# Kernel optimization log

Measured on AMD Instinct MI355X. Metric: run time of the kernel, lower is better.

## Reference

```python
import jax, jax.numpy as jnp
import numpy as np

NUM_HEADS = 8
CH_PER_HEAD = 32
NUM_GROUPS = 32
EPS = 1e-5
SCALE = CH_PER_HEAD ** (-0.25)


def setup_inputs() -> dict:
    key = jax.random.key(0)
    ks = jax.random.split(key, 6)
    B, C, H, W = 2, 256, 64, 64
    hid = NUM_HEADS * CH_PER_HEAD  # 256
    s = 1.0 / np.sqrt(C)
    return {
        "x": jax.random.normal(ks[0], (B, C, H, W), dtype=jnp.float32),
        "gamma": jnp.ones((C,), jnp.float32),
        "beta": jnp.zeros((C,), jnp.float32),
        "wq": jax.random.normal(ks[1], (hid, C), jnp.float32) * s,
        "bq": jnp.zeros((hid,), jnp.float32),
        "wk": jax.random.normal(ks[2], (hid, C), jnp.float32) * s,
        "bk": jnp.zeros((hid,), jnp.float32),
        "wv": jax.random.normal(ks[3], (hid, C), jnp.float32) * s,
        "bv": jnp.zeros((hid,), jnp.float32),
        "wout": jax.random.normal(ks[4], (C, hid), jnp.float32) * s,
        "bout": jnp.zeros((C,), jnp.float32),
    }


def _group_norm(x, gamma, beta):
    b, c, h, w = x.shape
    xg = x.reshape(b, NUM_GROUPS, c // NUM_GROUPS, h, w)
    mu = jnp.mean(xg, axis=(2, 3, 4), keepdims=True)
    var = jnp.var(xg, axis=(2, 3, 4), keepdims=True)
    xg = (xg - mu) * jax.lax.rsqrt(var + EPS)
    return xg.reshape(b, c, h, w) * gamma[None, :, None, None] + beta[None, :, None, None]


def reference(x, gamma, beta, wq, bq, wk, bk, wv, bv, wout, bout):
    b, c, h, w = x.shape
    n = h * w
    x_n = _group_norm(x, gamma, beta).reshape(b, c, n)  # b c n (self-attention: embedding = x_n)
    # 1x1 convs == pointwise linear over the channel dim
    q = jnp.einsum('oc,bcn->bon', wq, x_n) + bq[None, :, None]
    k = jnp.einsum('oc,bcn->bon', wk, x_n) + bk[None, :, None]
    v = jnp.einsum('oc,bcn->bon', wv, x_n) + bv[None, :, None]
    # split heads: b (h d) n -> b h d n
    d = CH_PER_HEAD
    q = q.reshape(b, NUM_HEADS, d, n)
    k = k.reshape(b, NUM_HEADS, d, n)
    v = v.reshape(b, NUM_HEADS, d, n)
    attn = jax.nn.softmax(jnp.einsum('bhdi,bhdj->bhij', q * SCALE, k * SCALE), axis=-1)
    out = jnp.einsum('bhij,bhdj->bhdi', attn, v).reshape(b, NUM_HEADS * d, n)
    out = jnp.einsum('oc,bcn->bon', wout, out) + bout[None, :, None]
    out = out.reshape(b, -1, h, w)
    return x + out  # shapes match -> residual
```

## Files before the change

### kernel.cpp

```cpp
#include <hip/hip_runtime.h>
#include <hip/hip_bf16.h>
#include <stdint.h>

typedef unsigned short u16;
typedef float f32x4 __attribute__((ext_vector_type(4)));
typedef float f32x16 __attribute__((ext_vector_type(16)));
typedef short bf16x8 __attribute__((ext_vector_type(8)));

#define NSP 4096
#define CDIM 256
#define HID 256
#define NH 8
#define DH 32
#define NG 32
#define CPG 8
#define BATCH 2
#define SPLIT 4
#define GN_EPS 1e-5f
#define QK2_SCALE 0.25503488f

#define MFMA32(A, B, C) __builtin_amdgcn_mfma_f32_32x32x16_bf16(A, B, C, 0, 0, 0)
#define MFMA16(A, B, C) __builtin_amdgcn_mfma_f32_16x16x32_bf16(A, B, C, 0, 0, 0)

__device__ __forceinline__ float bf2f(u16 u) {
    union { uint32_t i; float f; } v; v.i = ((uint32_t)u) << 16; return v.f;
}
__device__ __forceinline__ u16 f2bf(float f) {
    union { float f; uint32_t i; } v; v.f = f;
    uint32_t b = v.i;
    return (u16)((b + 0x7FFFu + ((b >> 16) & 1u)) >> 16);
}

__device__ __forceinline__ void gload16(const u16* g, u16* lds) {
    __builtin_amdgcn_global_load_lds(
        (const __attribute__((address_space(1))) uint32_t*)g,
        (__attribute__((address_space(3))) uint32_t*)lds, 16, 0, 0);
}

__device__ __forceinline__ void pl32swap(uint32_t& a, uint32_t& b) {
    asm("v_permlane32_swap_b32 %0, %1" : "+v"(a), "+v"(b));
}

__global__ void gn_stats(const float* __restrict__ x, float* __restrict__ stats,
                         const float* __restrict__ wq, const float* __restrict__ wk,
                         const float* __restrict__ wv, const float* __restrict__ wout,
                         u16* __restrict__ wcat) {
    int blk = blockIdx.x;
#pragma unroll
    for (int i = 0; i < 16; i++) {
        int idx = blk * 4096 + i * 256 + threadIdx.x;
        const float* src = (idx < 65536) ? wq : (idx < 131072) ? wk : (idx < 196608) ? wv : wout;
        wcat[idx] = f2bf(src[idx & 65535]);
    }
    const float4* base = (const float4*)(x + (size_t)blk * (CPG * NSP));
    float s = 0.f, ss = 0.f;
    for (int i = threadIdx.x; i < (CPG * NSP) / 4; i += 256) {
        float4 v = base[i];
        s  += v.x + v.y + v.z + v.w;
        ss += v.x * v.x + v.y * v.y + v.z * v.z + v.w * v.w;
    }
    for (int m = 1; m < 64; m <<= 1) { s += __shfl_xor(s, m, 64); ss += __shfl_xor(ss, m, 64); }
    __shared__ float ls[4], lss[4];
    int w = threadIdx.x >> 6;
    if ((threadIdx.x & 63) == 0) { ls[w] = s; lss[w] = ss; }
    __syncthreads();
    if (threadIdx.x == 0) {
        float S = ls[0] + ls[1] + ls[2] + ls[3];
        float SS = lss[0] + lss[1] + lss[2] + lss[3];
        float mean = S / (float)(CPG * NSP);
        float var = SS / (float)(CPG * NSP) - mean * mean;
        stats[2 * blk] = mean;
        stats[2 * blk + 1] = rsqrtf(var + GN_EPS);
    }
}

__global__ void gn_apply(const float* __restrict__ x, const float* __restrict__ stats,
                         const float* __restrict__ gamma, const float* __restrict__ beta,
                         u16* __restrict__ xn) {
    __shared__ u16 tile[64][72];
    int n0 = blockIdx.x * 64, c0 = blockIdx.y * 64, b = blockIdx.z;
    int t = threadIdx.x;
    int nl = t & 63, cq = t >> 6;
#pragma unroll
    for (int i = 0; i < 16; i++) {
        int cl = i * 4 + cq;
        int c = c0 + cl;
        int g = c >> 3;
        float mean = stats[2 * (b * NG + g)];
        float rstd = stats[2 * (b * NG + g) + 1];
        float v = x[((size_t)b * CDIM + c) * NSP + n0 + nl];
        v = (v - mean) * rstd * gamma[c] + beta[c];
        tile[cl][nl] = f2bf(v);
    }
    __syncthreads();
    int nr = t >> 2, cc = (t & 3) * 16;
    uint4 o0, o1;
    u16* p0 = (u16*)&o0; u16* p1 = (u16*)&o1;
#pragma unroll
    for (int j = 0; j < 8; j++) { p0[j] = tile[cc + j][nr]; p1[j] = tile[cc + 8 + j][nr]; }
    size_t orow = ((size_t)b * NSP + n0 + nr) * CDIM + c0 + cc;
    *(uint4*)(xn + orow) = o0;
    *(uint4*)(xn + orow + 8) = o1;
}

__global__ __launch_bounds__(256) void gemm_qkv(
    const u16* __restrict__ A, const u16* __restrict__ wcat,
    const float* __restrict__ bq, const float* __restrict__ bk, const float* __restrict__ bv,
    u16* __restrict__ qb, u16* __restrict__ kb, u16* __restrict__ vb) {
    __shared__ u16 As[128 * 64];
    __shared__ u16 Bs[128 * 64];
    int bz = blockIdx.z;
    const u16* Ab = A + (size_t)bz * NSP * CDIM;
    int n0 = blockIdx.x * 128, m0 = blockIdx.y * 128;
    int seg = n0 >> 8;
    int t = threadIdx.x, lane = t & 63, w = t >> 6;
    int wr = w >> 1, wc = w & 1;
    f32x4 acc[4][4] = {};

    int srow = w * 8 + (lane >> 3);
    int scol = (lane & 7) * 8;
    const u16* asrc = Ab + (size_t)(m0 + srow) * CDIM + scol;
    const u16* bsrc = wcat + (size_t)(n0 + srow) * CDIM + scol;
    u16* albase = As + w * 512;
    u16* blbase = Bs + w * 512;

    int frow = lane & 15, fcol = (lane >> 4) * 8;

    for (int k0 = 0; k0 < CDIM; k0 += 64) {
        __syncthreads();
#pragma unroll
        for (int ro = 0; ro < 4; ro++) {
            gload16(asrc + (size_t)ro * 32 * CDIM + k0, albase + ro * 2048);
            gload16(bsrc + (size_t)ro * 32 * CDIM + k0, blbase + ro * 2048);
        }
        asm volatile("s_waitcnt vmcnt(0)" ::: "memory");
        __syncthreads();
#pragma unroll
        for (int kk = 0; kk < 2; kk++) {
            bf16x8 af[4], bfv[4];
#pragma unroll
            for (int i = 0; i < 4; i++) {
                af[i]  = *(bf16x8*)&As[(wr * 64 + i * 16 + frow) * 64 + kk * 32 + fcol];
                bfv[i] = *(bf16x8*)&Bs[(wc * 64 + i * 16 + frow) * 64 + kk * 32 + fcol];
            }
#pragma unroll
            for (int i = 0; i < 4; i++)
#pragma unroll
                for (int j = 0; j < 4; j++)
                    acc[i][j] = MFMA16(af[i], bfv[j], acc[i][j]);
        }
    }

    const float* bias = (seg == 0) ? bq : (seg == 1) ? bk : bv;
    int r4 = (lane >> 4) * 4, cx = lane & 15;
#pragma unroll
    for (int i = 0; i < 4; i++) {
        int rbase = m0 + wr * 64 + i * 16 + r4;
#pragma unroll
        for (int j = 0; j < 4; j++) {
            int col = n0 + wc * 64 + j * 16 + cx;
            int cb = col & 255;
            float bb = bias[cb];
            if (seg == 0) {
#pragma unroll
                for (int r = 0; r < 4; r++)
                    qb[(size_t)bz * NSP * HID + (size_t)(rbase + r) * HID + cb] = f2bf(acc[i][j][r] + bb);
            } else if (seg == 1) {
#pragma unroll
                for (int r = 0; r < 4; r++)
                    kb[(size_t)bz * NSP * HID + (size_t)(rbase + r) * HID + cb] = f2bf((acc[i][j][r] + bb) * QK2_SCALE);
            } else {
                uint2 pkd;
                pkd.x = ((uint32_t)f2bf(acc[i][j][1] + bb) << 16) | f2bf(acc[i][j][0] + bb);
                pkd.y = ((uint32_t)f2bf(acc[i][j][3] + bb) << 16) | f2bf(acc[i][j][2] + bb);
                *(uint2*)(vb + (size_t)bz * HID * NSP + (size_t)cb * NSP + rbase) = pkd;
            }
        }
    }
}

__global__ __launch_bounds__(256) void gemm_out(
    const u16* __restrict__ A,
    const u16* __restrict__ B, long sB,
    const float* __restrict__ bias,
    const float* __restrict__ resid, long sR,
    float* __restrict__ outp, long sO,
    int N) {
    __shared__ u16 As[64][72];
    __shared__ u16 Bs[64][72];
    int bz = blockIdx.z;
    B += (size_t)bz * sB;
    int m0 = blockIdx.y * 64, n0 = blockIdx.x * 64;
    int t = threadIdx.x, lane = t & 63, w = t >> 6;
    int wm = (w >> 1) * 32, wn = (w & 1) * 32;
    f32x4 acc[2][2] = {};

    int sr = t >> 2;
    int sc1 = (t & 3) * 8, sc2 = sc1 + 32;

    uint4 av0 = *(const uint4*)(A + (size_t)(m0 + sr) * CDIM + sc1);
    uint4 av1 = *(const uint4*)(A + (size_t)(m0 + sr) * CDIM + sc2);
    uint4 bv0 = *(const uint4*)(B + (size_t)(n0 + sr) * CDIM + sc1);
    uint4 bv1 = *(const uint4*)(B + (size_t)(n0 + sr) * CDIM + sc2);

    for (int k0 = 0; k0 < CDIM; k0 += 64) {
        __syncthreads();
        *(uint4*)&As[sr][sc1] = av0;
        *(uint4*)&As[sr][sc2] = av1;
        *(uint4*)&Bs[sr][sc1] = bv0;
        *(uint4*)&Bs[sr][sc2] = bv1;
        __syncthreads();
        if (k0 + 64 < CDIM) {
            av0 = *(const uint4*)(A + (size_t)(m0 + sr) * CDIM + k0 + 64 + sc1);
            av1 = *(const uint4*)(A + (size_t)(m0 + sr) * CDIM + k0 + 64 + sc2);
            bv0 = *(const uint4*)(B + (size_t)(n0 + sr) * CDIM + k0 + 64 + sc1);
            bv1 = *(const uint4*)(B + (size_t)(n0 + sr) * CDIM + k0 + 64 + sc2);
        }
#pragma unroll
        for (int ks = 0; ks < 2; ks++) {
            bf16x8 af[2], bfr[2];
#pragma unroll
            for (int i = 0; i < 2; i++) {
                af[i]  = *(bf16x8*)&As[wm + i * 16 + (lane & 15)][ks * 32 + (lane >> 4) * 8];
                bfr[i] = *(bf16x8*)&Bs[wn + i * 16 + (lane & 15)][ks * 32 + (lane >> 4) * 8];
            }
#pragma unroll
            for (int i = 0; i < 2; i++)
#pragma unroll
                for (int j = 0; j < 2; j++)
                    acc[i][j] = MFMA16(af[i], bfr[j], acc[i][j]);
        }
    }

    int r4 = (lane >> 4) * 4, cx = lane & 15;
#pragma unroll
    for (int i = 0; i < 2; i++)
#pragma unroll
        for (int j = 0; j < 2; j++) {
            int rbase = m0 + wm + i * 16 + r4;
            int cbase = n0 + wn + j * 16 + cx;
#pragma unroll
            for (int r = 0; r < 4; r++) {
                int row = rbase + r, col = cbase;
                outp[(size_t)bz * sO + (size_t)row * N + col] =
                    acc[i][j][r] + bias[row] + resid[(size_t)bz * sR + (size_t)row * N + col];
            }
        }
}

__global__ __launch_bounds__(256, 2) void attn_kernel(
    const u16* __restrict__ q, const u16* __restrict__ k,
    const u16* __restrict__ v, u16* __restrict__ po, float* __restrict__ zz) {
    __shared__ u16 Ks[2][2048];
    __shared__ u16 Vs[2][2048];
    int h = blockIdx.y;
    int bz = blockIdx.z;
    int b = bz >> 2, sp = bz & 3;
    int kv0 = sp * (NSP / SPLIT);
    int t = threadIdx.x, lane = t & 63, w = t >> 6;
    int ql = lane & 31, hi = lane >> 5;
    int q0 = blockIdx.x * 256 + w * 64;

    const u16* qbp = q + (size_t)b * NSP * HID + (size_t)(q0 + ql) * HID + h * DH + hi * 8;
    bf16x8 qa0 = *(const bf16x8*)(qbp);
    bf16x8 qa1 = *(const bf16x8*)(qbp + 16);
    bf16x8 qb0 = *(const bf16x8*)(qbp + 32 * HID);
    bf16x8 qb1 = *(const bf16x8*)(qbp + 32 * HID + 16);

    int krow = t >> 2;
    int kslot = (t & 3) ^ ((krow >> 1) & 3);
    const u16* kg = k + (size_t)b * NSP * HID + (size_t)(kv0 + krow) * HID + h * DH + kslot * 8;
    int vd = t >> 3;
    int vg_ = (t & 7) ^ (vd & 7);
    const u16* vg = v + ((size_t)b * HID + h * DH + vd) * NSP + kv0 + vg_ * 8;
    const int wofs = w * 512;

    int kofs[4], vofs[4];
#pragma unroll
    for (int tt = 0; tt < 2; tt++) {
        int row = tt * 32 + ql;
        int sw = (row >> 1) & 3;
        kofs[2 * tt]     = row * 32 + ((hi ^ sw)) * 8;
        kofs[2 * tt + 1] = row * 32 + (((2 + hi) ^ sw)) * 8;
#pragma unroll
        for (int c = 0; c < 2; c++)
            vofs[2 * tt + c] = ql * 64 + (((4 * tt + 2 * c + hi) ^ (ql & 7))) * 8;
    }

    union { uint32_t u[4]; bf16x8 v8; } ones;
    ones.u[0] = 0x3F803F80u; ones.u[1] = 0x3F803F80u;
    ones.u[2] = 0x3F803F80u; ones.u[3] = 0x3F803F80u;

    f32x16 kzero = {};
    f32x16 oacc_a = {}, oacc_b = {};
    f32x16 lsum_a = {}, lsum_b = {};

    auto softpv = [&](f32x16& st, const u16* vp, int tt, f32x16& oacc, f32x16& lsum) {
        uint32_t pk[8];
#pragma unroll
        for (int j = 0; j < 8; j++) {
            float p0 = __builtin_amdgcn_exp2f(st[2 * j]);
            float p1 = __builtin_amdgcn_exp2f(st[2 * j + 1]);
            uint32_t dd;
            asm("v_cvt_pk_bf16_f32 %0, %1, %2" : "=v"(dd) : "v"(p0), "v"(p1));
            pk[j] = dd;
        }
#pragma unroll
        for (int c = 0; c < 2; c++) {
            uint32_t a0 = pk[4 * c + 0], b0 = pk[4 * c + 2];
            uint32_t a1 = pk[4 * c + 1], b1 = pk[4 * c + 3];
            pl32swap(a0, b0);
            pl32swap(a1, b1);
            union { uint32_t u[4]; bf16x8 v8; } fr;
            fr.u[0] = a0; fr.u[1] = a1; fr.u[2] = b0; fr.u[3] = b1;
            bf16x8 vf = *(const bf16x8*)(vp + vofs[2 * tt + c]);
            __builtin_amdgcn_s_setprio(1);
            oacc = MFMA32(fr.v8, vf, oacc);
            lsum = MFMA32(fr.v8, ones.v8, lsum);
            __builtin_amdgcn_s_setprio(0);
        }
    };

    auto process = [&](const u16* kp, const u16* vp) {
#pragma unroll
        for (int tt = 0; tt < 2; tt++) {
            bf16x8 kf0 = *(const bf16x8*)(kp + kofs[2 * tt]);
            bf16x8 kf1 = *(const bf16x8*)(kp + kofs[2 * tt + 1]);
            __builtin_amdgcn_s_setprio(1);
            f32x16 st_a = MFMA32(kf0, qa0, kzero);
            st_a = MFMA32(kf1, qa1, st_a);
            f32x16 st_b = MFMA32(kf0, qb0, kzero);
            st_b = MFMA32(kf1, qb1, st_b);
            __builtin_amdgcn_s_setprio(0);
            softpv(st_a, vp, tt, oacc_a, lsum_a);
            softpv(st_b, vp, tt, oacc_b, lsum_b);
        }
    };

    const int NT = (NSP / SPLIT) / 64;
    u16* kcur = Ks[0]; u16* knxt = Ks[1];
    u16* vcur = Vs[0]; u16* vnxt = Vs[1];
    gload16(kg, kcur + wofs); gload16(vg, vcur + wofs);
    kg += 64 * HID; vg += 64;
    asm volatile("s_waitcnt vmcnt(0)" ::: "memory");
    __syncthreads();
    for (int it = 0; it < NT; ++it) {
        if (it + 1 < NT) {
            gload16(kg, knxt + wofs); gload16(vg, vnxt + wofs);
            kg += 64 * HID; vg += 64;
        }
        process(kcur, vcur);
        asm volatile("s_waitcnt vmcnt(0)" ::: "memory");
        __syncthreads();
        u16* tp = kcur; kcur = knxt; knxt = tp;
        tp = vcur; vcur = vnxt; vnxt = tp;
    }

    float* zrow = zz + (((size_t)bz * NH + h) * NSP) + q0;
    if (ql == 0) {
#pragma unroll
        for (int r = 0; r < 16; r++) {
            int qq = (r & 3) + 8 * (r >> 2) + 4 * hi;
            zrow[qq] = __log2f(lsum_a[r]);
            zrow[32 + qq] = __log2f(lsum_b[r]);
        }
    }
    u16* pob = po + ((((size_t)bz * NH + h) * NSP) + q0) * DH + ql;
#pragma unroll
    for (int r = 0; r < 16; r++) {
        int qq = (r & 3) + 8 * (r >> 2) + 4 * hi;
        pob[(size_t)qq * DH] = f2bf(oacc_a[r] / lsum_a[r]);
        pob[(size_t)(32 + qq) * DH] = f2bf(oacc_b[r] / lsum_b[r]);
    }
}

__global__ __launch_bounds__(256) void combine_kernel(
    const u16* __restrict__ po, const float* __restrict__ zz, u16* __restrict__ ao) {
    int idx = blockIdx.x * 256 + threadIdx.x;
    int c8 = idx & 31;
    int n  = (idx >> 5) & (NSP - 1);
    int b  = idx >> 17;
    int h  = c8 >> 2;
    int dp = (c8 & 3) * 8;

    float z[SPLIT];
    size_t base[SPLIT];
    float M = -3e38f;
#pragma unroll
    for (int s = 0; s < SPLIT; s++) {
        base[s] = ((((size_t)(b * SPLIT + s) * NH + h) * NSP) + n);
        z[s] = zz[base[s]];
        M = fmaxf(M, z[s]);
    }
    float wsum = 0.f, acc[8] = {};
#pragma unroll
    for (int s = 0; s < SPLIT; s++) {
        float ww = __builtin_amdgcn_exp2f(z[s] - M);
        wsum += ww;
        uint4 o = *(const uint4*)(po + base[s] * DH + dp);
        const u16* op = (const u16*)&o;
#pragma unroll
        for (int j = 0; j < 8; j++) acc[j] += bf2f(op[j]) * ww;
    }
    float inv = 1.0f / wsum;
    uint4 r;
    u16* rp = (u16*)&r;
#pragma unroll
    for (int j = 0; j < 8; j++) rp[j] = f2bf(acc[j] * inv);
    *(uint4*)(ao + (((size_t)b * NSP + n) * HID) + h * DH + dp) = r;
}

extern "C" void kernel_launch(void* const* d_in, const int* in_sizes, int n_in,
                              void* d_out, int out_size, void* d_ws, size_t ws_size,
                              hipStream_t stream) {
    const float* x     = (const float*)d_in[0];
    const float* gamma = (const float*)d_in[1];
    const float* beta  = (const float*)d_in[2];
    const float* wq    = (const float*)d_in[3];
    const float* bq    = (const float*)d_in[4];
    const float* wk    = (const float*)d_in[5];
    const float* bk    = (const float*)d_in[6];
    const float* wv    = (const float*)d_in[7];
    const float* bv    = (const float*)d_in[8];
    const float* wout  = (const float*)d_in[9];
    const float* bout  = (const float*)d_in[10];
    float* out = (float*)d_out;

    char* ws = (char*)d_ws;
    float* stats = (float*)ws;
    u16* wq_b = (u16*)(ws + 4096);
    u16* wo_b = wq_b + 3 * 65536;
    u16* xn = wo_b + 65536;
    u16* qb = xn + (size_t)BATCH * NSP * CDIM;
    u16* kb = qb + (size_t)BATCH * NSP * HID;
    u16* vb = kb + (size_t)BATCH * NSP * HID;
    u16* aob = vb + (size_t)BATCH * HID * NSP;
    u16* pob = aob + (size_t)BATCH * NSP * HID;
    float* zzb = (float*)(pob + (size_t)SPLIT * BATCH * NH * NSP * DH);

    const long sQ = (long)NSP * HID;
    const long sOut = (long)CDIM * NSP;

    gn_stats<<<BATCH * NG, 256, 0, stream>>>(x, stats, wq, wk, wv, wout, wq_b);
    gn_apply<<<dim3(NSP / 64, CDIM / 64, BATCH), 256, 0, stream>>>(x, stats, gamma, beta, xn);

    gemm_qkv<<<dim3(768 / 128, NSP / 128, BATCH), 256, 0, stream>>>(
        xn, wq_b, bq, bk, bv, qb, kb, vb);

    attn_kernel<<<dim3(NSP / 256, NH, BATCH * SPLIT), 256, 0, stream>>>(qb, kb, vb, pob, zzb);
    combine_kernel<<<(BATCH * NSP * HID / 8) / 256, 256, 0, stream>>>(pob, zzb, aob);

    gemm_out<<<dim3(NSP / 64, CDIM / 64, BATCH), 256, 0, stream>>>(
        wo_b, aob, sQ, bout, x, sOut, out, sOut, NSP);
}
```

Measured before the change: 97.52 us.

## Pre-swizzle K/V into MFMA fragment layout and load directly to registers

The QKV GEMM epilogue now writes K and V in a tiled layout that matches the per-lane MFMA operand fragments of the attention kernel. The attention kernel drops its LDS double buffer, the barriers and the swizzle offset math, and instead loads each 64-key tile straight from global memory into registers with a two-deep software prefetch. This removes LDS traffic and block-wide synchronisation. In exchange, every wave now fetches the same K/V tile from global memory or cache, and the scattered epilogue stores in the GEMM may coalesce less well.

```diff
diff --git a/kernel.cpp b/kernel.cpp
--- a/kernel.cpp
+++ b/kernel.cpp
@@ -106,7 +106,7 @@
 __global__ __launch_bounds__(256) void gemm_qkv(
     const u16* __restrict__ A, const u16* __restrict__ wcat,
     const float* __restrict__ bq, const float* __restrict__ bk, const float* __restrict__ bv,
-    u16* __restrict__ qb, u16* __restrict__ kb, u16* __restrict__ vb) {
+    u16* __restrict__ qb, u16* __restrict__ kfb, u16* __restrict__ vfb) {
     __shared__ u16 As[128 * 64];
     __shared__ u16 Bs[128 * 64];
     int bz = blockIdx.z;
@@ -166,14 +166,22 @@
                 for (int r = 0; r < 4; r++)
                     qb[(size_t)bz * NSP * HID + (size_t)(rbase + r) * HID + cb] = f2bf(acc[i][j][r] + bb);
             } else if (seg == 1) {
+                int h2 = cb >> 5;
+                int f = 2 * ((rbase >> 5) & 1) + ((cb >> 4) & 1);
+                size_t kt = ((size_t)(bz * NH + h2) * 64 + (rbase >> 6)) * 2048
+                          + (size_t)f * 512 + ((rbase & 31) + (((cb >> 3) & 1) << 5)) * 8 + (cb & 7);
 #pragma unroll
                 for (int r = 0; r < 4; r++)
-                    kb[(size_t)bz * NSP * HID + (size_t)(rbase + r) * HID + cb] = f2bf((acc[i][j][r] + bb) * QK2_SCALE);
+                    kfb[kt + r * 8] = f2bf((acc[i][j][r] + bb) * QK2_SCALE);
             } else {
+                int h2 = cb >> 5, d = cb & 31;
+                int jc = (rbase >> 3) & 7;
+                size_t vt = ((size_t)(bz * NH + h2) * 64 + (rbase >> 6)) * 2048
+                          + (size_t)(jc >> 1) * 512 + (d + ((jc & 1) << 5)) * 8 + (rbase & 7);
                 uint2 pkd;
                 pkd.x = ((uint32_t)f2bf(acc[i][j][1] + bb) << 16) | f2bf(acc[i][j][0] + bb);
                 pkd.y = ((uint32_t)f2bf(acc[i][j][3] + bb) << 16) | f2bf(acc[i][j][2] + bb);
-                *(uint2*)(vb + (size_t)bz * HID * NSP + (size_t)cb * NSP + rbase) = pkd;
+                *(uint2*)(vfb + vt) = pkd;
             }
         }
     }
@@ -249,10 +257,8 @@
 }
 
 __global__ __launch_bounds__(256, 2) void attn_kernel(
-    const u16* __restrict__ q, const u16* __restrict__ k,
-    const u16* __restrict__ v, u16* __restrict__ po, float* __restrict__ zz) {
-    __shared__ u16 Ks[2][2048];
-    __shared__ u16 Vs[2][2048];
+    const u16* __restrict__ q, const u16* __restrict__ kfb,
+    const u16* __restrict__ vfb, u16* __restrict__ po, float* __restrict__ zz) {
     int h = blockIdx.y;
     int bz = blockIdx.z;
     int b = bz >> 2, sp = bz & 3;
@@ -267,25 +273,19 @@
     bf16x8 qb0 = *(const bf16x8*)(qbp + 32 * HID);
     bf16x8 qb1 = *(const bf16x8*)(qbp + 32 * HID + 16);
 
-    int krow = t >> 2;
-    int kslot = (t & 3) ^ ((krow >> 1) & 3);
-    const u16* kg = k + (size_t)b * NSP * HID + (size_t)(kv0 + krow) * HID + h * DH + kslot * 8;
-    int vd = t >> 3;
-    int vg_ = (t & 7) ^ (vd & 7);
-    const u16* vg = v + ((size_t)b * HID + h * DH + vd) * NSP + kv0 + vg_ * 8;
-    const int wofs = w * 512;
-
-    int kofs[4], vofs[4];
-#pragma unroll
-    for (int tt = 0; tt < 2; tt++) {
-        int row = tt * 32 + ql;
-        int sw = (row >> 1) & 3;
-        kofs[2 * tt]     = row * 32 + ((hi ^ sw)) * 8;
-        kofs[2 * tt + 1] = row * 32 + (((2 + hi) ^ sw)) * 8;
-#pragma unroll
-        for (int c = 0; c < 2; c++)
-            vofs[2 * tt + c] = ql * 64 + (((4 * tt + 2 * c + hi) ^ (ql & 7))) * 8;
-    }
+    size_t tbase = ((size_t)(b * NH + h) * 64 + (kv0 >> 6)) * 2048 + (size_t)lane * 8;
+    const u16* kp = kfb + tbase;
+    const u16* vp = vfb + tbase;
+
+#define LOADT(kd, vd, it) { \
+    kd[0] = *(const bf16x8*)(kp + (size_t)(it) * 2048);        \
+    kd[1] = *(const bf16x8*)(kp + (size_t)(it) * 2048 + 512);  \
+    kd[2] = *(const bf16x8*)(kp + (size_t)(it) * 2048 + 1024); \
+    kd[3] = *(const bf16x8*)(kp + (size_t)(it) * 2048 + 1536); \
+    vd[0] = *(const bf16x8*)(vp + (size_t)(it) * 2048);        \
+    vd[1] = *(const bf16x8*)(vp + (size_t)(it) * 2048 + 512);  \
+    vd[2] = *(const bf16x8*)(vp + (size_t)(it) * 2048 + 1024); \
+    vd[3] = *(const bf16x8*)(vp + (size_t)(it) * 2048 + 1536); }
 
     union { uint32_t u[4]; bf16x8 v8; } ones;
     ones.u[0] = 0x3F803F80u; ones.u[1] = 0x3F803F80u;
@@ -295,7 +295,7 @@
     f32x16 oacc_a = {}, oacc_b = {};
     f32x16 lsum_a = {}, lsum_b = {};
 
-    auto softpv = [&](f32x16& st, const u16* vp, int tt, f32x16& oacc, f32x16& lsum) {
+    auto softpv = [&](f32x16& st, const bf16x8 (&vf)[4], int tt, f32x16& oacc, f32x16& lsum) {
         uint32_t pk[8];
 #pragma unroll
         for (int j = 0; j < 8; j++) {
@@ -313,48 +313,39 @@
             pl32swap(a1, b1);
             union { uint32_t u[4]; bf16x8 v8; } fr;
             fr.u[0] = a0; fr.u[1] = a1; fr.u[2] = b0; fr.u[3] = b1;
-            bf16x8 vf = *(const bf16x8*)(vp + vofs[2 * tt + c]);
             __builtin_amdgcn_s_setprio(1);
-            oacc = MFMA32(fr.v8, vf, oacc);
+            oacc = MFMA32(fr.v8, vf[2 * tt + c], oacc);
             lsum = MFMA32(fr.v8, ones.v8, lsum);
             __builtin_amdgcn_s_setprio(0);
         }
     };
 
-    auto process = [&](const u16* kp, const u16* vp) {
+    auto process = [&](const bf16x8 (&kf)[4], const bf16x8 (&vf)[4]) {
 #pragma unroll
         for (int tt = 0; tt < 2; tt++) {
-            bf16x8 kf0 = *(const bf16x8*)(kp + kofs[2 * tt]);
-            bf16x8 kf1 = *(const bf16x8*)(kp + kofs[2 * tt + 1]);
             __builtin_amdgcn_s_setprio(1);
-            f32x16 st_a = MFMA32(kf0, qa0, kzero);
-            st_a = MFMA32(kf1, qa1, st_a);
-            f32x16 st_b = MFMA32(kf0, qb0, kzero);
-            st_b = MFMA32(kf1, qb1, st_b);
+            f32x16 st_a = MFMA32(kf[2 * tt], qa0, kzero);
+            st_a = MFMA32(kf[2 * tt + 1], qa1, st_a);
+            f32x16 st_b = MFMA32(kf[2 * tt], qb0, kzero);
+            st_b = MFMA32(kf[2 * tt + 1], qb1, st_b);
             __builtin_amdgcn_s_setprio(0);
-            softpv(st_a, vp, tt, oacc_a, lsum_a);
-            softpv(st_b, vp, tt, oacc_b, lsum_b);
+            softpv(st_a, vf, tt, oacc_a, lsum_a);
+            softpv(st_b, vf, tt, oacc_b, lsum_b);
         }
     };
 
     const int NT = (NSP / SPLIT) / 64;
-    u16* kcur = Ks[0]; u16* knxt = Ks[1];
-    u16* vcur = Vs[0]; u16* vnxt = Vs[1];
-    gload16(kg, kcur + wofs); gload16(vg, vcur + wofs);
-    kg += 64 * HID; vg += 64;
-    asm volatile("s_waitcnt vmcnt(0)" ::: "memory");
-    __syncthreads();
-    for (int it = 0; it < NT; ++it) {
-        if (it + 1 < NT) {
-            gload16(kg, knxt + wofs); gload16(vg, vnxt + wofs);
-            kg += 64 * HID; vg += 64;
-        }
-        process(kcur, vcur);
-        asm volatile("s_waitcnt vmcnt(0)" ::: "memory");
-        __syncthreads();
-        u16* tp = kcur; kcur = knxt; knxt = tp;
-        tp = vcur; vcur = vnxt; vnxt = tp;
-    }
+    bf16x8 ka[4], va[4], kc[4], vc[4];
+    LOADT(ka, va, 0);
+    for (int it = 0; it < NT; it += 2) {
+        int n1 = (it + 1 < NT) ? it + 1 : 0;
+        LOADT(kc, vc, n1);
+        process(ka, va);
+        int n2 = (it + 2 < NT) ? it + 2 : 0;
+        LOADT(ka, va, n2);
+        process(kc, vc);
+    }
+#undef LOADT
 
     float* zrow = zz + (((size_t)bz * NH + h) * NSP) + q0;
     if (ql == 0) {
@@ -432,9 +423,9 @@
     u16* wo_b = wq_b + 3 * 65536;
     u16* xn = wo_b + 65536;
     u16* qb = xn + (size_t)BATCH * NSP * CDIM;
-    u16* kb = qb + (size_t)BATCH * NSP * HID;
-    u16* vb = kb + (size_t)BATCH * NSP * HID;
-    u16* aob = vb + (size_t)BATCH * HID * NSP;
+    u16* kfb = qb + (size_t)BATCH * NSP * HID;
+    u16* vfb = kfb + (size_t)BATCH * NH * 64 * 2048;
+    u16* aob = vfb + (size_t)BATCH * NH * 64 * 2048;
     u16* pob = aob + (size_t)BATCH * NSP * HID;
     float* zzb = (float*)(pob + (size_t)SPLIT * BATCH * NH * NSP * DH);
 
@@ -445,9 +436,9 @@
     gn_apply<<<dim3(NSP / 64, CDIM / 64, BATCH), 256, 0, stream>>>(x, stats, gamma, beta, xn);
 
     gemm_qkv<<<dim3(768 / 128, NSP / 128, BATCH), 256, 0, stream>>>(
-        xn, wq_b, bq, bk, bv, qb, kb, vb);
-
-    attn_kernel<<<dim3(NSP / 256, NH, BATCH * SPLIT), 256, 0, stream>>>(qb, kb, vb, pob, zzb);
+        xn, wq_b, bq, bk, bv, qb, kfb, vfb);
+
+    attn_kernel<<<dim3(NSP / 256, NH, BATCH * SPLIT), 256, 0, stream>>>(qb, kfb, vfb, pob, zzb);
     combine_kernel<<<(BATCH * NSP * HID / 8) / 256, 256, 0, stream>>>(pob, zzb, aob);
 
     gemm_out<<<dim3(NSP / 64, CDIM / 64, BATCH), 256, 0, stream>>>(
```

Result: faster. 93.84 us (-3.8%).
